# Optimization experiments

Hardware: AMD Instinct MI355X
Metric: run time of the kernel (lower is better)

The kernel has to match this reference:

```python
import math
import jax, jax.numpy as jnp
import numpy as np

L, B, S, D, HID, NH = 4, 2, 2048, 1024, 1024, 16
C = HID // NH  # 64


def setup_inputs() -> dict:
    key = jax.random.key(0)
    ks = jax.random.split(key, 8)
    p = lambda k, shape: jax.random.normal(k, shape, jnp.float32) * 0.02
    return {
        "x": jax.random.normal(ks[0], (B, S, D), jnp.float32),
        "Wq": p(ks[1], (L, D, HID)), "bq": jnp.zeros((L, HID), jnp.float32),
        "Wk": p(ks[2], (L, D, HID)), "bk": jnp.zeros((L, HID), jnp.float32),
        "Wv": p(ks[3], (L, D, HID)), "bv": jnp.zeros((L, HID), jnp.float32),
        "Wo": p(ks[4], (L, HID, D)), "bo": jnp.zeros((L, D), jnp.float32),
        "W1": p(ks[5], (L, D, HID)), "b1": jnp.zeros((L, HID), jnp.float32),
        "W2": p(ks[6], (L, HID, D)), "b2": jnp.zeros((L, D), jnp.float32),
        "gamma": jnp.ones((L, D), jnp.float32),   # single LayerNorm reused twice per block
        "beta": jnp.zeros((L, D), jnp.float32),
    }


def _pos_enc(seq_len, d, n=1000.0):
    col = jnp.arange(seq_len, dtype=jnp.float32)[:, None]        # [S,1]
    row = jnp.arange(d)                                          # [D]
    exp = (2.0 * (row // 2).astype(jnp.float32)) / d
    mat = col / jnp.power(n, exp)[None, :]                       # [S,D]
    return jnp.where(row % 2 == 0, jnp.sin(mat), jnp.cos(mat))


def _layernorm(x, g, b, eps=1e-5):
    mu = jnp.mean(x, axis=-1, keepdims=True)
    var = jnp.mean((x - mu) ** 2, axis=-1, keepdims=True)        # biased, as torch
    return (x - mu) / jnp.sqrt(var + eps) * g + b


def _block(x, Wq, bq, Wk, bk, Wv, bv, Wo, bo, W1, b1, W2, b2, g, be):
    b_, s_, _ = x.shape
    q = ((x @ Wq + bq)).reshape(b_, s_, NH, C) / math.sqrt(C)
    k = (x @ Wk + bk).reshape(b_, s_, NH, C)
    v = (x @ Wv + bv).reshape(b_, s_, NH, C)
    # NOTE: faithful to original einsum '...hq,...hk->...hqk' -> per-token
    # attention over the CHANNEL axis c, with a (c,c) causal mask.
    aff = jnp.einsum('bshq,bshk->bshqk', q, k)                   # [B,S,H,C,C]
    mask = jnp.triu(jnp.ones((C, C), bool), 1)
    aff = jnp.where(mask, -jnp.inf, aff)
    w = jax.nn.softmax(aff, axis=-1)
    av = jnp.einsum('bshqk,bshk->bshq', w, v).reshape(b_, s_, HID)
    attn_out = av @ Wo + bo
    x = _layernorm(attn_out + x, g, be)
    mlp_out = jax.nn.relu(x @ W1 + b1) @ W2 + b2
    return _layernorm(mlp_out + x, g, be)


def reference(x, Wq, bq, Wk, bk, Wv, bv, Wo, bo, W1, b1, W2, b2, gamma, beta):
    x = x + _pos_enc(x.shape[1], x.shape[2])
    for i in range(L):
        x = _block(x, Wq[i], bq[i], Wk[i], bk[i], Wv[i], bv[i], Wo[i], bo[i],
                   W1[i], b1[i], W2[i], b2[i], gamma[i], beta[i])
    return x
```

## Files before the change

### kernel.cpp

```cpp
#include <hip/hip_runtime.h>
#include <hip/hip_bf16.h>
#include <stdint.h>

#define TOK 4096
#define DM  1024

using u16 = unsigned short;
typedef __attribute__((ext_vector_type(8))) short short8;
typedef __attribute__((ext_vector_type(4))) float f32x4;

__device__ __forceinline__ u16 f2bf(float f){
  unsigned u = __float_as_uint(f);
  return (u16)((u + 0x7fffu + ((u >> 16) & 1u)) >> 16);
}
__device__ __forceinline__ float bf2f(u16 h){ return __uint_as_float(((unsigned)h) << 16); }

__device__ __forceinline__ float fexp2(float x){
#if __has_builtin(__builtin_amdgcn_exp2f)
  return __builtin_amdgcn_exp2f(x);
#else
  float r; asm("v_exp_f32 %0, %1\n\ts_nop 0" : "=v"(r) : "v"(x)); return r;
#endif
}

__global__ __launch_bounds__(256) void posenc_add(
    const float* __restrict__ x, float* __restrict__ r, u16* __restrict__ xb)
{
  const int t = blockIdx.x;
  const int s = t & 2047;
  const size_t base = (size_t)t * DM;
#pragma unroll
  for (int i = 0; i < 4; ++i){
    const int d = threadIdx.x + i * 256;
    const float e = (float)(d & ~1) * (1.0f / (float)DM);
    const float denom = powf(1000.0f, e);
    const float mat = (float)s / denom;
    const float pe = (d & 1) ? cosf(mat) : sinf(mat);
    const float v = x[base + d] + pe;
    r[base + d] = v;
    xb[base + d] = f2bf(v);
  }
}

__global__ __launch_bounds__(256) void transpose6(
    const float* __restrict__ Wq, const float* __restrict__ Wk, const float* __restrict__ Wv,
    const float* __restrict__ Wo, const float* __restrict__ W1, const float* __restrict__ W2,
    u16* __restrict__ WT, int l0)
{
  __shared__ float tile[32][33];
  const int bid = blockIdx.x;
  const int l  = l0 + bid / 6144;
  const int mm = (bid >> 10) % 6;
  const int t  = bid & 1023;
  const int tn = (t & 31) * 32;
  const int tk = (t >> 5) * 32;
  const float* src = (mm==0)?Wq:(mm==1)?Wk:(mm==2)?Wv:(mm==3)?Wo:(mm==4)?W1:W2;
  src += (size_t)l * 1048576;
  u16* dst = WT + ((size_t)(l - l0) * 6 + mm) * 1048576;
  const int tx = threadIdx.x & 31, ty = threadIdx.x >> 5;
#pragma unroll
  for (int i = 0; i < 4; ++i)
    tile[ty + i*8][tx] = src[(size_t)(tk + ty + i*8) * 1024 + tn + tx];
  __syncthreads();
#pragma unroll
  for (int i = 0; i < 4; ++i)
    dst[(size_t)(tn + ty + i*8) * 1024 + tk + tx] = f2bf(tile[tx][ty + i*8]);
}

#define BM 128
#define BK 64
#define KD 1024

template<int MODE, int BNt>
__global__ __launch_bounds__(256) void gemm_k1024(
    const u16* __restrict__ A, const u16* __restrict__ BT,
    const float* __restrict__ bias0, const float* __restrict__ bias1, const float* __restrict__ bias2,
    u16* __restrict__ outB, int M, int N)
{
  constexpr int NFR = BNt / 32;
  __shared__ __align__(16) u16 sA[BM*BK];
  __shared__ __align__(16) u16 sB[BNt*BK];
  const int tid  = threadIdx.x;
  const int lane = tid & 63;
  const int wave = tid >> 6;
  const int nbn = N / BNt;
  const int nwg = gridDim.x;
  const int wg  = (blockIdx.x & 7) * (nwg >> 3) + (blockIdx.x >> 3);
  const size_t m0 = (size_t)(wg / nbn) * BM;
  const size_t n0 = (size_t)(wg % nbn) * BNt;

  const int srow  = lane >> 3;
  const int sslot = (lane & 7) ^ srow;
  const u16* gA = A  + (m0 + wave*32 + srow) * KD + sslot * 8;
  const u16* gB = BT + (n0 + wave*(BNt/4) + srow) * KD + sslot * 8;
  u16* lA = sA + (wave*32) * 64;
  u16* lB = sB + (wave*(BNt/4)) * 64;

  const int wm = (wave >> 1) * 64;
  const int wn = (wave & 1) * (BNt/2);
  f32x4 acc[4][NFR] = {};

  for (int kt = 0; kt < KD/BK; ++kt){
    const int k0 = kt * BK;
#pragma unroll
    for (int p = 0; p < 4; ++p)
      __builtin_amdgcn_global_load_lds(
          (const __attribute__((address_space(1))) void*)(gA + p*8*KD + k0),
          (__attribute__((address_space(3))) void*)(lA + p*8*64), 16, 0, 0);
#pragma unroll
    for (int p = 0; p < BNt/32; ++p)
      __builtin_amdgcn_global_load_lds(
          (const __attribute__((address_space(1))) void*)(gB + p*8*KD + k0),
          (__attribute__((address_space(3))) void*)(lB + p*8*64), 16, 0, 0);
    __syncthreads();
#pragma unroll
    for (int kk = 0; kk < 2; ++kk){
      short8 af[4], bfr[NFR];
      const int kidx = kk*4 + (lane >> 4);
#pragma unroll
      for (int i = 0; i < 4; ++i){
        const int arow = wm + i*16 + (lane & 15);
        af[i]  = *(const short8*)(sA + arow*64 + (kidx ^ (arow & 7)) * 8);
      }
#pragma unroll
      for (int j = 0; j < NFR; ++j){
        const int brow = wn + j*16 + (lane & 15);
        bfr[j] = *(const short8*)(sB + brow*64 + (kidx ^ (brow & 7)) * 8);
      }
#pragma unroll
      for (int i = 0; i < 4; ++i)
#pragma unroll
        for (int j = 0; j < NFR; ++j)
          acc[i][j] = __builtin_amdgcn_mfma_f32_16x16x32_bf16(af[i], bfr[j], acc[i][j], 0, 0, 0);
    }
    __syncthreads();
  }

#pragma unroll
  for (int i = 0; i < 4; ++i){
    const int growb = wm + i*16 + (lane >> 4) * 4;
#pragma unroll
    for (int j = 0; j < NFR; ++j){
      const size_t gcol = n0 + wn + j*16 + (lane & 15);
      float bv;
      if constexpr (MODE == 2)
        bv = (gcol < 1024) ? bias0[gcol] : (gcol < 2048) ? bias1[gcol - 1024] : bias2[gcol - 2048];
      else
        bv = bias0[gcol];
#pragma unroll
      for (int r = 0; r < 4; ++r){
        const size_t grow = m0 + growb + r;
        float v = acc[i][j][r] + bv;
        if constexpr (MODE == 0)      outB[grow * N + gcol] = f2bf(v);
        else if constexpr (MODE == 1) outB[grow * N + gcol] = f2bf(fmaxf(v, 0.0f));
        else                          outB[grow * N + gcol] = f2bf(gcol < 1024 ? v * 0.125f : v);
      }
    }
  }
}

__global__ __launch_bounds__(256) void attn_chan(
    const u16* __restrict__ qkv, u16* __restrict__ av)
{
  __shared__ __align__(16) float2 skv[4][64];
  const int t    = blockIdx.x >> 2;
  const int hb   = blockIdx.x & 3;
  const int lane = threadIdx.x & 63;
  const int wave = threadIdx.x >> 6;
  const int h    = hb * 4 + wave;
  float2* kw = skv[wave];
  const int r = lane & 3;
  const size_t base = (size_t)t * 3072 + h * 64 + lane;
  const float qi2 = bf2f(qkv[base]) * 1.44269504f;
  const float ki  = bf2f(qkv[base + 1024]);
  const float vi  = bf2f(qkv[base + 2048]);
  kw[lane] = make_float2(ki, vi);
  float ssum = 0.0f, acc = 0.0f;
#pragma unroll 8
  for (int j0 = 0; j0 < 64; j0 += 4){
    const float4 ab = *(const float4*)(kw + j0);
    const float4 cd = *(const float4*)(kw + j0 + 2);
    const float bias = (j0 + 3 <= lane) ? 0.0f : -200.0f;
    const float e0 = fexp2(fmaf(qi2, ab.x, bias));
    const float e1 = fexp2(fmaf(qi2, ab.z, bias));
    const float e2 = fexp2(fmaf(qi2, cd.x, bias));
    const float e3 = fexp2(fmaf(qi2, cd.z, bias));
    ssum += (e0 + e1) + (e2 + e3);
    acc = fmaf(e0, ab.y, acc);
    acc = fmaf(e1, ab.w, acc);
    acc = fmaf(e2, cd.y, acc);
    acc = fmaf(e3, cd.w, acc);
  }
#pragma unroll
  for (int s = 0; s < 3; ++s){
    const float2 kv = kw[lane - r + s];
    const float bf = (s <= r && r < 3) ? 0.0f : -200.0f;
    const float e = fexp2(fmaf(qi2, kv.x, bf));
    ssum += e;
    acc = fmaf(e, kv.y, acc);
  }
  av[(size_t)t * 1024 + h * 64 + lane] = f2bf(acc / ssum);
}

__global__ __launch_bounds__(256) void residual_ln(
    const u16* __restrict__ y, const float* xres,
    const float* __restrict__ gamma, const float* __restrict__ beta,
    float* xout, u16* __restrict__ xb)
{
  __shared__ float red[4];
  const int row = blockIdx.x, tid = threadIdx.x;
  const int lane = tid & 63, wave = tid >> 6;
  const ushort4 a = ((const ushort4*)(y + (size_t)row*DM))[tid];
  const float4  b = ((const float4*)(xres + (size_t)row*DM))[tid];
  float4 s; s.x=bf2f(a.x)+b.x; s.y=bf2f(a.y)+b.y; s.z=bf2f(a.z)+b.z; s.w=bf2f(a.w)+b.w;
  float p = s.x + s.y + s.z + s.w;
#pragma unroll
  for (int o = 32; o; o >>= 1) p += __shfl_xor(p, o);
  if (lane == 0) red[wave] = p;
  __syncthreads();
  const float mu = (red[0]+red[1]+red[2]+red[3]) * (1.0f/(float)DM);
  __syncthreads();
  const float dx=s.x-mu, dy=s.y-mu, dz=s.z-mu, dw=s.w-mu;
  float q2 = dx*dx + dy*dy + dz*dz + dw*dw;
#pragma unroll
  for (int o = 32; o; o >>= 1) q2 += __shfl_xor(q2, o);
  if (lane == 0) red[wave] = q2;
  __syncthreads();
  const float var = (red[0]+red[1]+red[2]+red[3]) * (1.0f/(float)DM);
  const float rstd = rsqrtf(var + 1e-5f);
  const float4 g  = ((const float4*)gamma)[tid];
  const float4 be = ((const float4*)beta)[tid];
  float4 o4;
  o4.x = dx*rstd*g.x + be.x;
  o4.y = dy*rstd*g.y + be.y;
  o4.z = dz*rstd*g.z + be.z;
  o4.w = dw*rstd*g.w + be.w;
  ((float4*)(xout + (size_t)row*DM))[tid] = o4;
  ushort4 ob; ob.x=f2bf(o4.x); ob.y=f2bf(o4.y); ob.z=f2bf(o4.z); ob.w=f2bf(o4.w);
  ((ushort4*)(xb + (size_t)row*DM))[tid] = ob;
}

extern "C" void kernel_launch(void* const* d_in, const int* in_sizes, int n_in,
                              void* d_out, int out_size, void* d_ws, size_t ws_size,
                              hipStream_t stream)
{
  const float* x    = (const float*)d_in[0];
  const float* Wq   = (const float*)d_in[1];
  const float* bq   = (const float*)d_in[2];
  const float* Wk   = (const float*)d_in[3];
  const float* bk   = (const float*)d_in[4];
  const float* Wv   = (const float*)d_in[5];
  const float* bv   = (const float*)d_in[6];
  const float* Wo   = (const float*)d_in[7];
  const float* bo   = (const float*)d_in[8];
  const float* W1   = (const float*)d_in[9];
  const float* b1   = (const float*)d_in[10];
  const float* W2   = (const float*)d_in[11];
  const float* b2   = (const float*)d_in[12];
  const float* gam  = (const float*)d_in[13];
  const float* bet  = (const float*)d_in[14];

  char* ws = (char*)d_ws;
  size_t off = 0;
  auto alloc = [&](size_t b){ void* p = ws + off; off = (off + b + 255) & ~(size_t)255; return p; };

  const size_t oneWT = 6ull*1048576*2;
  const size_t rest  = ((size_t)TOK*DM*4)
                     + ((size_t)TOK*DM*2)
                     + ((size_t)TOK*3072*2)
                     + ((size_t)TOK*DM*2)
                     + ((size_t)TOK*DM*2)
                     + ((size_t)TOK*DM*2)
                     + 4096;
  const bool all4 = (4*oneWT + rest) <= ws_size;

  u16*   WT   = (u16*)  alloc(all4 ? 4*oneWT : oneWT);
  float* res  = (float*)alloc((size_t)TOK*DM*4);
  u16*   xb   = (u16*)  alloc((size_t)TOK*DM*2);
  u16*   qkv  = (u16*)  alloc((size_t)TOK*3072*2);
  u16*   avb  = (u16*)  alloc((size_t)TOK*DM*2);
  u16*   hbuf = (u16*)  alloc((size_t)TOK*DM*2);
  u16*   ybuf = (u16*)  alloc((size_t)TOK*DM*2);
  if (off > ws_size) return;

  posenc_add<<<TOK, 256, 0, stream>>>(x, res, xb);
  if (all4)
    transpose6<<<4*6*1024, 256, 0, stream>>>(Wq, Wk, Wv, Wo, W1, W2, WT, 0);

  for (int l = 0; l < 4; ++l){
    u16* wt = all4 ? (WT + (size_t)l * 6 * 1048576) : WT;
    if (!all4)
      transpose6<<<6*1024, 256, 0, stream>>>(Wq, Wk, Wv, Wo, W1, W2, WT, l);
    gemm_k1024<2,128><<<(TOK/BM)*(3072/128), 256, 0, stream>>>(
        xb, wt, bq + l*1024, bk + l*1024, bv + l*1024, qkv, TOK, 3072);
    attn_chan<<<TOK*4, 256, 0, stream>>>(qkv, avb);
    gemm_k1024<0,64><<<(TOK/BM)*(1024/64), 256, 0, stream>>>(
        avb, wt + 3ull*1048576, bo + l*1024, nullptr, nullptr, ybuf, TOK, 1024);
    residual_ln<<<TOK, 256, 0, stream>>>(ybuf, res, gam + l*1024, bet + l*1024, res, xb);
    gemm_k1024<1,64><<<(TOK/BM)*(1024/64), 256, 0, stream>>>(
        xb, wt + 4ull*1048576, b1 + l*1024, nullptr, nullptr, hbuf, TOK, 1024);
    gemm_k1024<0,64><<<(TOK/BM)*(1024/64), 256, 0, stream>>>(
        hbuf, wt + 5ull*1048576, b2 + l*1024, nullptr, nullptr, ybuf, TOK, 1024);
    float* xdst = (l == 3) ? (float*)d_out : res;
    residual_ln<<<TOK, 256, 0, stream>>>(ybuf, res, gam + l*1024, bet + l*1024, xdst, xb);
  }
}
```

Baseline: 618.2 us.

## Fuse QKV projection GEMM with per-token channel attention in one kernel

Each new workgroup computes the Q, K and V projection for 128 tokens and one head as a 128x192 tile held in LDS, then runs the per-token channel softmax attention straight from LDS. This drops the separate attention kernel and the global round trip through the bf16 qkv buffer. The softmax division becomes a hardware reciprocal approximation. The trade-offs are a narrower 192-column GEMM tile with 512 threads, which may lower MFMA efficiency or occupancy, and a serial attention epilogue after the matmul.

```diff
diff --git a/kernel.cpp b/kernel.cpp
--- a/kernel.cpp
+++ b/kernel.cpp
@@ -20,6 +20,13 @@
   return __builtin_amdgcn_exp2f(x);
 #else
   float r; asm("v_exp_f32 %0, %1\n\ts_nop 0" : "=v"(r) : "v"(x)); return r;
+#endif
+}
+__device__ __forceinline__ float frcp(float x){
+#if __has_builtin(__builtin_amdgcn_rcpf)
+  return __builtin_amdgcn_rcpf(x);
+#else
+  float r; asm("v_rcp_f32 %0, %1\n\ts_nop 0" : "=v"(r) : "v"(x)); return r;
 #endif
 }
 
@@ -71,10 +78,144 @@
 #define BK 64
 #define KD 1024
 
+#define QS 200
+
+__global__ __launch_bounds__(512, 4) void qkv_attn(
+    const u16* __restrict__ A, const u16* __restrict__ WTq,
+    const float* __restrict__ bq, const float* __restrict__ bk, const float* __restrict__ bv,
+    u16* __restrict__ av)
+{
+  __shared__ __align__(16) u16 lds[128 * QS];
+  u16* sA = lds;
+  u16* sB = lds + 8192;
+  const int tid  = threadIdx.x;
+  const int lane = tid & 63;
+  const int wave = tid >> 6;
+  const int nwg = gridDim.x;
+  const int wg  = (blockIdx.x & 7) * (nwg >> 3) + (blockIdx.x >> 3);
+  const int h   = wg & 15;
+  const int t0  = (wg >> 4) * BM;
+
+  const int srow  = lane >> 3;
+  const int sslot = (lane & 7) ^ srow;
+  const u16* gA = A + (size_t)(t0 + wave*16 + srow) * KD + sslot * 8;
+  u16* lA = sA + (wave*2) * 512;
+  const int c0 = wave * 3;
+  const u16* gB0 = WTq + (size_t)((c0+0)>>3)*1048576 + (size_t)(h*64 + ((c0+0)&7)*8 + srow)*KD + sslot*8;
+  const u16* gB1 = WTq + (size_t)((c0+1)>>3)*1048576 + (size_t)(h*64 + ((c0+1)&7)*8 + srow)*KD + sslot*8;
+  const u16* gB2 = WTq + (size_t)((c0+2)>>3)*1048576 + (size_t)(h*64 + ((c0+2)&7)*8 + srow)*KD + sslot*8;
+  u16* lB0 = sB + (c0+0) * 512;
+  u16* lB1 = sB + (c0+1) * 512;
+  u16* lB2 = sB + (c0+2) * 512;
+
+  const int wr = wave >> 2;
+  const int wc = wave & 3;
+  f32x4 acc[4][3] = {};
+
+  for (int kt = 0; kt < KD/BK; ++kt){
+    const int k0 = kt * BK;
+#pragma unroll
+    for (int p = 0; p < 2; ++p)
+      __builtin_amdgcn_global_load_lds(
+          (const __attribute__((address_space(1))) void*)(gA + p*8*KD + k0),
+          (__attribute__((address_space(3))) void*)(lA + p*512), 16, 0, 0);
+    __builtin_amdgcn_global_load_lds(
+        (const __attribute__((address_space(1))) void*)(gB0 + k0),
+        (__attribute__((address_space(3))) void*)lB0, 16, 0, 0);
+    __builtin_amdgcn_global_load_lds(
+        (const __attribute__((address_space(1))) void*)(gB1 + k0),
+        (__attribute__((address_space(3))) void*)lB1, 16, 0, 0);
+    __builtin_amdgcn_global_load_lds(
+        (const __attribute__((address_space(1))) void*)(gB2 + k0),
+        (__attribute__((address_space(3))) void*)lB2, 16, 0, 0);
+    __syncthreads();
+#pragma unroll
+    for (int kk = 0; kk < 2; ++kk){
+      short8 af[4], bfr[3];
+      const int kidx = kk*4 + (lane >> 4);
+#pragma unroll
+      for (int i = 0; i < 4; ++i){
+        const int arow = wr*64 + i*16 + (lane & 15);
+        af[i] = *(const short8*)(sA + arow*64 + (kidx ^ (arow & 7)) * 8);
+      }
+#pragma unroll
+      for (int j = 0; j < 3; ++j){
+        const int brow = wc*48 + j*16 + (lane & 15);
+        bfr[j] = *(const short8*)(sB + brow*64 + (kidx ^ (brow & 7)) * 8);
+      }
+#pragma unroll
+      for (int i = 0; i < 4; ++i)
+#pragma unroll
+        for (int j = 0; j < 3; ++j)
+          acc[i][j] = __builtin_amdgcn_mfma_f32_16x16x32_bf16(af[i], bfr[j], acc[i][j], 0, 0, 0);
+    }
+    __syncthreads();
+  }
+
+#pragma unroll
+  for (int i = 0; i < 4; ++i){
+    const int row = wr*64 + i*16 + (lane >> 4) * 4;
+#pragma unroll
+    for (int j = 0; j < 3; ++j){
+      const int col = wc*48 + j*16 + (lane & 15);
+      float bias;
+      if (col < 64)       bias = bq[h*64 + col];
+      else if (col < 128) bias = bk[h*64 + col - 64];
+      else                bias = bv[h*64 + col - 128];
+      const bool isq = (col < 64);
+#pragma unroll
+      for (int r = 0; r < 4; ++r){
+        float v = acc[i][j][r] + bias;
+        if (isq) v *= 0.125f;
+        lds[(row + r) * QS + col] = f2bf(v);
+      }
+    }
+  }
+  __syncthreads();
+
+  const int r3 = lane & 3;
+  for (int tt = 0; tt < 16; tt += 2){
+    const int ta = wave*16 + tt;
+    const u16* rowa = lds + ta * QS;
+    const u16* rowb = rowa + QS;
+    const float qa = bf2f(rowa[lane]) * 1.44269504f;
+    const float qb = bf2f(rowb[lane]) * 1.44269504f;
+    float sa = 0.f, aa = 0.f, sb = 0.f, ab = 0.f;
+#pragma unroll
+    for (int j0 = 0; j0 < 64; j0 += 8){
+      const short8 ka = *(const short8*)(rowa + 64 + j0);
+      const short8 va = *(const short8*)(rowa + 128 + j0);
+      const short8 kb = *(const short8*)(rowb + 64 + j0);
+      const short8 vb = *(const short8*)(rowb + 128 + j0);
+      const float bias0 = (j0 + 3 <= lane) ? 0.0f : -200.0f;
+      const float bias1 = (j0 + 7 <= lane) ? 0.0f : -200.0f;
+#pragma unroll
+      for (int q = 0; q < 8; ++q){
+        const float bias = (q < 4) ? bias0 : bias1;
+        const float ea = fexp2(fmaf(qa, bf2f((u16)ka[q]), bias));
+        const float eb = fexp2(fmaf(qb, bf2f((u16)kb[q]), bias));
+        sa += ea; aa = fmaf(ea, bf2f((u16)va[q]), aa);
+        sb += eb; ab = fmaf(eb, bf2f((u16)vb[q]), ab);
+      }
+    }
+#pragma unroll
+    for (int s = 0; s < 3; ++s){
+      const int jj = lane - r3 + s;
+      const float bias = (s <= r3 && r3 < 3) ? 0.0f : -200.0f;
+      const float ea = fexp2(fmaf(qa, bf2f(rowa[64 + jj]), bias));
+      const float eb = fexp2(fmaf(qb, bf2f(rowb[64 + jj]), bias));
+      sa += ea; aa = fmaf(ea, bf2f(rowa[128 + jj]), aa);
+      sb += eb; ab = fmaf(eb, bf2f(rowb[128 + jj]), ab);
+    }
+    av[(size_t)(t0 + ta)     * DM + h*64 + lane] = f2bf(aa * frcp(sa));
+    av[(size_t)(t0 + ta + 1) * DM + h*64 + lane] = f2bf(ab * frcp(sb));
+  }
+}
+
 template<int MODE, int BNt>
 __global__ __launch_bounds__(256) void gemm_k1024(
     const u16* __restrict__ A, const u16* __restrict__ BT,
-    const float* __restrict__ bias0, const float* __restrict__ bias1, const float* __restrict__ bias2,
+    const float* __restrict__ bias0,
     u16* __restrict__ outB, int M, int N)
 {
   constexpr int NFR = BNt / 32;
@@ -142,64 +283,16 @@
 #pragma unroll
     for (int j = 0; j < NFR; ++j){
       const size_t gcol = n0 + wn + j*16 + (lane & 15);
-      float bv;
-      if constexpr (MODE == 2)
-        bv = (gcol < 1024) ? bias0[gcol] : (gcol < 2048) ? bias1[gcol - 1024] : bias2[gcol - 2048];
-      else
-        bv = bias0[gcol];
+      const float bv = bias0[gcol];
 #pragma unroll
       for (int r = 0; r < 4; ++r){
         const size_t grow = m0 + growb + r;
         float v = acc[i][j][r] + bv;
-        if constexpr (MODE == 0)      outB[grow * N + gcol] = f2bf(v);
-        else if constexpr (MODE == 1) outB[grow * N + gcol] = f2bf(fmaxf(v, 0.0f));
-        else                          outB[grow * N + gcol] = f2bf(gcol < 1024 ? v * 0.125f : v);
-      }
-    }
-  }
-}
-
-__global__ __launch_bounds__(256) void attn_chan(
-    const u16* __restrict__ qkv, u16* __restrict__ av)
-{
-  __shared__ __align__(16) float2 skv[4][64];
-  const int t    = blockIdx.x >> 2;
-  const int hb   = blockIdx.x & 3;
-  const int lane = threadIdx.x & 63;
-  const int wave = threadIdx.x >> 6;
-  const int h    = hb * 4 + wave;
-  float2* kw = skv[wave];
-  const int r = lane & 3;
-  const size_t base = (size_t)t * 3072 + h * 64 + lane;
-  const float qi2 = bf2f(qkv[base]) * 1.44269504f;
-  const float ki  = bf2f(qkv[base + 1024]);
-  const float vi  = bf2f(qkv[base + 2048]);
-  kw[lane] = make_float2(ki, vi);
-  float ssum = 0.0f, acc = 0.0f;
-#pragma unroll 8
-  for (int j0 = 0; j0 < 64; j0 += 4){
-    const float4 ab = *(const float4*)(kw + j0);
-    const float4 cd = *(const float4*)(kw + j0 + 2);
-    const float bias = (j0 + 3 <= lane) ? 0.0f : -200.0f;
-    const float e0 = fexp2(fmaf(qi2, ab.x, bias));
-    const float e1 = fexp2(fmaf(qi2, ab.z, bias));
-    const float e2 = fexp2(fmaf(qi2, cd.x, bias));
-    const float e3 = fexp2(fmaf(qi2, cd.z, bias));
-    ssum += (e0 + e1) + (e2 + e3);
-    acc = fmaf(e0, ab.y, acc);
-    acc = fmaf(e1, ab.w, acc);
-    acc = fmaf(e2, cd.y, acc);
-    acc = fmaf(e3, cd.w, acc);
-  }
-#pragma unroll
-  for (int s = 0; s < 3; ++s){
-    const float2 kv = kw[lane - r + s];
-    const float bf = (s <= r && r < 3) ? 0.0f : -200.0f;
-    const float e = fexp2(fmaf(qi2, kv.x, bf));
-    ssum += e;
-    acc = fmaf(e, kv.y, acc);
-  }
-  av[(size_t)t * 1024 + h * 64 + lane] = f2bf(acc / ssum);
+        if constexpr (MODE == 1) v = fmaxf(v, 0.0f);
+        outB[grow * N + gcol] = f2bf(v);
+      }
+    }
+  }
 }
 
 __global__ __launch_bounds__(256) void residual_ln(
@@ -267,7 +360,6 @@
   const size_t oneWT = 6ull*1048576*2;
   const size_t rest  = ((size_t)TOK*DM*4)
                      + ((size_t)TOK*DM*2)
-                     + ((size_t)TOK*3072*2)
                      + ((size_t)TOK*DM*2)
                      + ((size_t)TOK*DM*2)
                      + ((size_t)TOK*DM*2)
@@ -277,7 +369,6 @@
   u16*   WT   = (u16*)  alloc(all4 ? 4*oneWT : oneWT);
   float* res  = (float*)alloc((size_t)TOK*DM*4);
   u16*   xb   = (u16*)  alloc((size_t)TOK*DM*2);
-  u16*   qkv  = (u16*)  alloc((size_t)TOK*3072*2);
   u16*   avb  = (u16*)  alloc((size_t)TOK*DM*2);
   u16*   hbuf = (u16*)  alloc((size_t)TOK*DM*2);
   u16*   ybuf = (u16*)  alloc((size_t)TOK*DM*2);
@@ -291,16 +382,15 @@
     u16* wt = all4 ? (WT + (size_t)l * 6 * 1048576) : WT;
     if (!all4)
       transpose6<<<6*1024, 256, 0, stream>>>(Wq, Wk, Wv, Wo, W1, W2, WT, l);
-    gemm_k1024<2,128><<<(TOK/BM)*(3072/128), 256, 0, stream>>>(
-        xb, wt, bq + l*1024, bk + l*1024, bv + l*1024, qkv, TOK, 3072);
-    attn_chan<<<TOK*4, 256, 0, stream>>>(qkv, avb);
+    qkv_attn<<<(TOK/BM)*16, 512, 0, stream>>>(
+        xb, wt, bq + l*1024, bk + l*1024, bv + l*1024, avb);
     gemm_k1024<0,64><<<(TOK/BM)*(1024/64), 256, 0, stream>>>(
-        avb, wt + 3ull*1048576, bo + l*1024, nullptr, nullptr, ybuf, TOK, 1024);
+        avb, wt + 3ull*1048576, bo + l*1024, ybuf, TOK, 1024);
     residual_ln<<<TOK, 256, 0, stream>>>(ybuf, res, gam + l*1024, bet + l*1024, res, xb);
     gemm_k1024<1,64><<<(TOK/BM)*(1024/64), 256, 0, stream>>>(
-        xb, wt + 4ull*1048576, b1 + l*1024, nullptr, nullptr, hbuf, TOK, 1024);
+        xb, wt + 4ull*1048576, b1 + l*1024, hbuf, TOK, 1024);
     gemm_k1024<0,64><<<(TOK/BM)*(1024/64), 256, 0, stream>>>(
-        hbuf, wt + 5ull*1048576, b2 + l*1024, nullptr, nullptr, ybuf, TOK, 1024);
+        hbuf, wt + 5ull*1048576, b2 + l*1024, ybuf, TOK, 1024);
     float* xdst = (l == 3) ? (float*)d_out : res;
     residual_ln<<<TOK, 256, 0, stream>>>(ybuf, res, gam + l*1024, bet + l*1024, xdst, xb);
   }
```

Result: no change. 621.8 us (+0.6%).
